# Kernel tuning notes

Hardware: AMD Instinct MI355X
Metric: run time of the kernel (lower is better)

The kernel has to match this reference:

```python
import jax, jax.numpy as jnp
import numpy as np

N = 10000      # atoms
E = 160000     # edges (avg degree 16)
H = 64         # hidden_channels
R = 64         # num_rbf
MAXZ = 100
RC = 4.5       # cutoff_upper (cutoff_lower = 0)
LN_EPS = 1e-5


def setup_inputs() -> dict:
    key = jax.random.key(0)
    ks = jax.random.split(key, 20)
    z = jax.random.randint(ks[0], (N,), 0, MAXZ, dtype=jnp.int32)
    edge_index = jax.random.randint(ks[1], (2, E), 0, N, dtype=jnp.int32)
    edge_weight = jax.random.uniform(ks[2], (E,), dtype=jnp.float32) * RC
    v = jax.random.normal(ks[3], (E, 3), dtype=jnp.float32)
    edge_vec_norm = v / jnp.linalg.norm(v, axis=-1, keepdims=True)
    edge_attr = jax.random.normal(ks[4], (E, R), dtype=jnp.float32)
    p = lambda k, shape: (jax.random.normal(k, shape, dtype=jnp.float32) * 0.1)
    return {
        'z': z, 'edge_index': edge_index, 'edge_weight': edge_weight,
        'edge_vec_norm': edge_vec_norm, 'edge_attr': edge_attr,
        'emb': p(ks[5], (MAXZ, H)),
        'emb2_w': p(ks[6], (H, 2 * H)), 'emb2_b': p(ks[7], (H,)),
        'dp1_w': p(ks[8], (H, R)), 'dp1_b': p(ks[9], (H,)),
        'dp2_w': p(ks[10], (H, R)), 'dp2_b': p(ks[11], (H,)),
        'dp3_w': p(ks[12], (H, R)), 'dp3_b': p(ks[13], (H,)),
        'ln_g': jnp.ones((H,), jnp.float32), 'ln_b': jnp.zeros((H,), jnp.float32),
        'w1': p(ks[14], (2 * H, H)), 'b1': jnp.zeros((2 * H,), jnp.float32),
        'w2': p(ks[15], (3 * H, 2 * H)), 'b2': jnp.zeros((3 * H,), jnp.float32),
        'm0': p(ks[16], (H, H)), 'm1': p(ks[17], (H, H)), 'm2': p(ks[18], (H, H)),
    }


def reference(z, edge_index, edge_weight, edge_vec_norm, edge_attr,
              emb, emb2_w, emb2_b, dp1_w, dp1_b, dp2_w, dp2_b, dp3_w, dp3_b,
              ln_g, ln_b, w1, b1, w2, b2, m0, m1, m2):
    n_atoms = z.shape[0]
    hc = emb.shape[1]
    src, dst = edge_index[0], edge_index[1]

    # atomic number message Z_ij: concat(Z_i, Z_j) -> Linear  [E,H]
    Zn = emb[z]
    Zij = jnp.concatenate([Zn[src], Zn[dst]], axis=-1) @ emb2_w.T + emb2_b

    # cosine cutoff (cutoff_lower == 0)
    C = 0.5 * (jnp.cos(edge_weight * jnp.pi / RC) + 1.0) * (edge_weight < RC)

    # RBF-gated per-edge channel weights, all [E,H]
    g1 = (edge_attr @ dp1_w.T + dp1_b) * C[:, None] * Zij
    g2 = (edge_attr @ dp2_w.T + dp2_b) * C[:, None] * Zij
    g3 = (edge_attr @ dp3_w.T + dp3_b) * C[:, None] * Zij

    eye = jnp.eye(3, dtype=Zij.dtype)
    vx, vy, vz = edge_vec_norm[:, 0], edge_vec_norm[:, 1], edge_vec_norm[:, 2]
    zero = jnp.zeros_like(vx)
    skew = jnp.stack([zero, -vz, vy, vz, zero, -vx, -vy, vx, zero], axis=-1).reshape(-1, 3, 3)
    outer = edge_vec_norm[:, :, None] * edge_vec_norm[:, None, :]  # [E,3,3], symmetric
    sym = outer - (jnp.trace(outer, axis1=-2, axis2=-1) / 3.0)[:, None, None] * eye

    # per-edge messages [E,H,3,3]
    Iij = g1[:, :, None, None] * eye
    Aij = g2[:, :, None, None] * skew[:, None, :, :]
    Sij = g3[:, :, None, None] * sym[:, None, :, :]

    # scatter-add to atoms
    I = jax.ops.segment_sum(Iij, src, num_segments=n_atoms)
    A = jax.ops.segment_sum(Aij, src, num_segments=n_atoms)
    S = jax.ops.segment_sum(Sij, src, num_segments=n_atoms)

    # tensor norm -> layernorm -> MLP1
    tn = ((I + A + S) ** 2).sum((-2, -1))  # [N,H]
    mu = tn.mean(-1, keepdims=True)
    var = ((tn - mu) ** 2).mean(-1, keepdims=True)
    norm = (tn - mu) / jnp.sqrt(var + LN_EPS) * ln_g + ln_b
    norm = jax.nn.silu(norm @ w1.T + b1)
    norm = jax.nn.silu(norm @ w2.T + b2)
    norm = norm.reshape(-1, hc, 3)
    n0 = norm[..., 0][:, :, None, None]

    # channel-mixing; NOTE: original code applies MLP2[1]/MLP2[2] to the
    # updated I and gates all three with norm[...,0] -- replicated faithfully.
    I = jnp.einsum('nhij,kh->nkij', I, m0) * n0
    A = jnp.einsum('nhij,kh->nkij', I, m1) * n0
    S = jnp.einsum('nhij,kh->nkij', I, m2) * n0
    return I + A + S
```

## Files before the change

### kernel.cpp

```cpp
#include <hip/hip_runtime.h>
#include <stdint.h>

#define NATOMS 10000
#define NEDGES 160000
#define RCUT   4.5f
#define CAP    64
#define ATGRID 1024

#define T_BYTES    ((size_t)NATOMS * 640 * 4)
#define CNT_OFF    (T_BYTES)
#define CNT_BYTES  ((size_t)NATOMS * 4)
#define REC_OFF    (CNT_OFF + CNT_BYTES)
#define REC_BYTES  ((size_t)NATOMS * CAP * 16)
#define EMB_OFF    (REC_OFF + REC_BYTES)
#define EMB_BYTES  ((size_t)100 * 64 * 2)
#define ATTR2_OFF  (EMB_OFF + 0x4000)
#define ATTR2_BYTES ((size_t)NATOMS * CAP * 64 * 2)
#define WS_NEED    (ATTR2_OFF + ATTR2_BYTES)

typedef unsigned short u16;
typedef __bf16 bf16x8 __attribute__((ext_vector_type(8)));
typedef float  f32x4  __attribute__((ext_vector_type(4)));

#define MFMA16(a,b,c) __builtin_amdgcn_mfma_f32_16x16x32_bf16((a),(b),(c),0,0,0)
#define BFMAGIC 0x3F803F80u
#define MSK 0xffff0000u

__device__ __forceinline__ float uf(unsigned int u){ return __uint_as_float(u); }
__device__ __forceinline__ float b2f(u16 u){
  union { unsigned int i; float f; } v; v.i = ((unsigned int)u) << 16; return v.f;
}
__device__ __forceinline__ u16 f2b(float f){
  union { unsigned int i; float f; } v; v.f = f;
  unsigned int b = v.i + 0x7fffu + ((v.i >> 16) & 1u);
  return (u16)(b >> 16);
}
__device__ __forceinline__ float ldf(const void* p, int i, int bf){
  if (bf) return b2f(((const u16*)p)[i]);
  return ((const float*)p)[i];
}
__device__ __forceinline__ bf16x8 ld8bf(const void* p, int i, int bf){
  if (bf) return *(const bf16x8*)((const u16*)p + i);
  const float4* q = (const float4*)((const float*)p + i);
  float4 a = q[0], b = q[1];
  bf16x8 r;
  r[0]=(__bf16)a.x; r[1]=(__bf16)a.y; r[2]=(__bf16)a.z; r[3]=(__bf16)a.w;
  r[4]=(__bf16)b.x; r[5]=(__bf16)b.y; r[6]=(__bf16)b.z; r[7]=(__bf16)b.w;
  return r;
}
__device__ __forceinline__ uint4 ld8pk(const void* p, int i, int bf){
  if (bf) return *(const uint4*)((const u16*)p + i);
  const float4* q = (const float4*)((const float*)p + i);
  float4 a = q[0], b = q[1];
  uint4 r;
  r.x = (unsigned int)f2b(a.x) | ((unsigned int)f2b(a.y) << 16);
  r.y = (unsigned int)f2b(a.z) | ((unsigned int)f2b(a.w) << 16);
  r.z = (unsigned int)f2b(b.x) | ((unsigned int)f2b(b.y) << 16);
  r.w = (unsigned int)f2b(b.z) | ((unsigned int)f2b(b.w) << 16);
  return r;
}
__device__ __forceinline__ void ld8f(const void* p, int i, float* o, int bf){
  if (bf){
    uint4 v = *(const uint4*)((const u16*)p + i);
    o[0]=uf(v.x<<16); o[1]=uf(v.x&MSK); o[2]=uf(v.y<<16); o[3]=uf(v.y&MSK);
    o[4]=uf(v.z<<16); o[5]=uf(v.z&MSK); o[6]=uf(v.w<<16); o[7]=uf(v.w&MSK);
    return;
  }
  const float4* q = (const float4*)((const float*)p + i);
  float4 a = q[0], b = q[1];
  o[0]=a.x; o[1]=a.y; o[2]=a.z; o[3]=a.w; o[4]=b.x; o[5]=b.y; o[6]=b.z; o[7]=b.w;
}
__device__ __forceinline__ uint4 pk8(const float* f){
  uint4 r;
  r.x = (unsigned int)f2b(f[0]) | ((unsigned int)f2b(f[1]) << 16);
  r.y = (unsigned int)f2b(f[2]) | ((unsigned int)f2b(f[3]) << 16);
  r.z = (unsigned int)f2b(f[4]) | ((unsigned int)f2b(f[5]) << 16);
  r.w = (unsigned int)f2b(f[6]) | ((unsigned int)f2b(f[7]) << 16);
  return r;
}

__global__ __launch_bounds__(256) void scatter_kernel(const int* __restrict__ ei,
                                                      const int* __restrict__ z,
                                                      const void* __restrict__ ew,
                                                      const void* __restrict__ evn,
                                                      const void* __restrict__ emb,
                                                      u16* __restrict__ emb16,
                                                      int* __restrict__ cnt,
                                                      uint4* __restrict__ REC,
                                                      const void* __restrict__ attr,
                                                      u16* __restrict__ attr2,
                                                      const unsigned int* __restrict__ lng){
  const int bf = (lng[0] == BFMAGIC);
  int e = blockIdx.x * 256 + threadIdx.x;
  if (e < 6400) emb16[e] = bf ? ((const u16*)emb)[e] : f2b(((const float*)emb)[e]);
  int s = ei[e], d = ei[NEDGES + e];
  int p = atomicAdd(&cnt[s], 1);
  const float w  = ldf(ew, e, bf);
  const float Cv = (w < RCUT) ? 0.5f*(__cosf(w * (3.14159265358979f / RCUT)) + 1.0f) : 0.0f;
  uint4 rec;
  rec.x = (unsigned int)e;
  rec.y = (unsigned int)z[d];
  rec.z = (unsigned int)f2b(ldf(evn, 3*e + 0, bf)) | ((unsigned int)f2b(ldf(evn, 3*e + 1, bf)) << 16);
  rec.w = (unsigned int)f2b(ldf(evn, 3*e + 2, bf)) | ((unsigned int)f2b(Cv) << 16);
  if (p < CAP){
    REC[(size_t)s*CAP + p] = rec;
    if (attr2){
      u16* dst = attr2 + ((size_t)s*CAP + p)*64;
#pragma unroll
      for (int k = 0; k < 8; k++)
        *(uint4*)(dst + k*8) = ld8pk(attr, e*64 + k*8, bf);
    }
  }
}

__global__ __launch_bounds__(256)
void atomT_stream(
    const int* __restrict__ z,
    const u16* __restrict__ emb16,
    const u16* __restrict__ attr2,
    const uint4* __restrict__ REC,
    const int* __restrict__ cnt,
    const void* __restrict__ e2w, const void* __restrict__ e2b,
    const void* __restrict__ d1w, const void* __restrict__ d1b,
    const void* __restrict__ d2w, const void* __restrict__ d2b,
    const void* __restrict__ d3w, const void* __restrict__ d3b,
    float* __restrict__ T,
    const unsigned int* __restrict__ lng)
{
  __shared__ __align__(16) u16 dpW[3][64][64];
  __shared__ __align__(16) u16 e2W[64][128];

  const int bf  = (lng[0] == BFMAGIC);
  const int tid = threadIdx.x;
  const void* dps[3] = {d1w, d2w, d3w};
  for (int idx = tid; idx < 1536; idx += 256){
    int w = idx >> 9, rem = idx & 511, r = rem >> 3, c8 = rem & 7;
    *(bf16x8*)&dpW[w][r][(c8 ^ (r & 7))*8] = ld8bf(dps[w], r*64 + c8*8, bf);
  }
  for (int idx = tid; idx < 1024; idx += 256){
    int r = idx >> 4, c8 = idx & 15;
    *(bf16x8*)&e2W[r][(c8 ^ (r & 7))*8] = ld8bf(e2w, r*128 + c8*8, bf);
  }
  __syncthreads();

  const int lane = tid & 63;
  const int wave = tid >> 6;
  const int hh   = lane & 15;
  const int quad = lane >> 4;
  const int half = wave & 1;
  const int ntb  = half * 2;
  const int wpair = wave >> 1;

  float be2[2], bd1[2], bd2[2], bd3[2];
#pragma unroll
  for (int j = 0; j < 2; j++){
    int h = hh + 16*(ntb + j);
    be2[j] = ldf(e2b, h, bf); bd1[j] = ldf(d1b, h, bf);
    bd2[j] = ldf(d2b, h, bf); bd3[j] = ldf(d3b, h, bf);
  }

  int pr  = blockIdx.x;
  int n   = pr * 2 + wpair;
  int cn  = cnt[n];
  int zsv = z[n];

  while (true) {
    const int e0   = n * CAP;
    const int nv   = min(cn, CAP);
    const int e1   = e0 + nv;
    const int e1m1 = (nv > 0) ? (e1 - 1) : e0;
    uint4 recA = REC[min(e0 + hh, e1m1)];

    bf16x8 zf0 = *(const bf16x8*)(emb16 + zsv*64 + quad*8);
    bf16x8 zf1 = *(const bf16x8*)(emb16 + zsv*64 + 32 + quad*8);

    const int prn  = pr + ATGRID;
    const bool more = (prn < NATOMS/2);
    const int nn   = prn * 2 + wpair;
    if (more){ cn = cnt[nn]; zsv = z[nn]; }

    float P[10][2];
#pragma unroll
    for (int c = 0; c < 10; c++){ P[c][0] = 0.f; P[c][1] = 0.f; }

    for (int base = e0; base < e1; base += 16){
      const size_t sA = (size_t)min(base + hh, e1 - 1) * 64;
      bf16x8 af0 = *(const bf16x8*)(attr2 + sA + quad*8);
      bf16x8 af1 = *(const bf16x8*)(attr2 + sA + 32 + quad*8);

      uint4 recN = REC[min(base + 16 + hh, e1 - 1)];

      bf16x8 zf2 = *(const bf16x8*)(emb16 + recA.y*64 + quad*8);
      bf16x8 zf3 = *(const bf16x8*)(emb16 + recA.y*64 + 32 + quad*8);

      f32x4 aZ[2], a1[2], a2[2], a3[2];
#pragma unroll
      for (int j = 0; j < 2; j++){
        aZ[j] = (f32x4){0.f,0.f,0.f,0.f};
        a1[j] = (f32x4){0.f,0.f,0.f,0.f};
        a2[j] = (f32x4){0.f,0.f,0.f,0.f};
        a3[j] = (f32x4){0.f,0.f,0.f,0.f};
      }

#pragma unroll
      for (int j = 0; j < 2; j++){
        const int h  = hh + 16*(ntb + j);
        const int s0 = (quad       ^ (h & 7)) * 8;
        const int s1 = ((quad + 4) ^ (h & 7)) * 8;
        bf16x8 b;
        b = *(const bf16x8*)&dpW[0][h][s0];           a1[j] = MFMA16(af0, b, a1[j]);
        b = *(const bf16x8*)&dpW[0][h][s1];           a1[j] = MFMA16(af1, b, a1[j]);
        b = *(const bf16x8*)&dpW[1][h][s0];           a2[j] = MFMA16(af0, b, a2[j]);
        b = *(const bf16x8*)&dpW[1][h][s1];           a2[j] = MFMA16(af1, b, a2[j]);
        b = *(const bf16x8*)&dpW[2][h][s0];           a3[j] = MFMA16(af0, b, a3[j]);
        b = *(const bf16x8*)&dpW[2][h][s1];           a3[j] = MFMA16(af1, b, a3[j]);
        b = *(const bf16x8*)&e2W[h][s0];              aZ[j] = MFMA16(zf0, b, aZ[j]);
        b = *(const bf16x8*)&e2W[h][s1];              aZ[j] = MFMA16(zf1, b, aZ[j]);
        b = *(const bf16x8*)&e2W[h][((quad + 8)  ^ (h & 7)) * 8];  aZ[j] = MFMA16(zf2, b, aZ[j]);
        b = *(const bf16x8*)&e2W[h][((quad + 12) ^ (h & 7)) * 8];  aZ[j] = MFMA16(zf3, b, aZ[j]);
      }

#pragma unroll
      for (int r = 0; r < 4; r++){
        const int ii = base + quad*4 + r;
        const bool ea = (ii < e1);
        const int srcl = quad*20 + r;
        const unsigned int rz = (unsigned int)__shfl((int)recA.z, srcl, 64);
        const unsigned int rw = (unsigned int)__shfl((int)recA.w, srcl, 64);
        const float Cv = ea ? b2f((u16)(rw >> 16)) : 0.f;
        const float vx = b2f((u16)(rz & 0xffffu));
        const float vy = b2f((u16)(rz >> 16));
        const float vz = b2f((u16)(rw & 0xffffu));
        const float xx = vx*vx - (1.f/3.f), yy = vy*vy - (1.f/3.f), zz = vz*vz - (1.f/3.f);
        const float xy = vx*vy, xz = vx*vz, yz = vy*vz;
#pragma unroll
        for (int j = 0; j < 2; j++){
          const float czv = Cv * (aZ[j][r] + be2[j]);
          const float g1 = (a1[j][r] + bd1[j]) * czv;
          const float g2 = (a2[j][r] + bd2[j]) * czv;
          const float g3 = (a3[j][r] + bd3[j]) * czv;
          P[0][j] += g1;
          P[1][j] += g2*vx; P[2][j] += g2*vy; P[3][j] += g2*vz;
          P[4][j] += g3*xx; P[5][j] += g3*yy; P[6][j] += g3*zz;
          P[7][j] += g3*xy; P[8][j] += g3*xz; P[9][j] += g3*yz;
        }
      }
      recA = recN;
    }

#pragma unroll
    for (int c = 0; c < 10; c++)
#pragma unroll
      for (int j = 0; j < 2; j++){
        float v = P[c][j];
        v += __shfl_xor(v, 16, 64);
        v += __shfl_xor(v, 32, 64);
        P[c][j] = v;
      }

    if ((quad >> 1) == half){
      float* Tn = T + (size_t)n * 640;
#pragma unroll
      for (int c = 0; c < 10; c++)
        Tn[c*64 + lane] = P[c][quad & 1];
    }

    if (!more) break;
    pr = prn; n = nn;
  }
}

__global__ __launch_bounds__(256)
void atomT_kernel(
    const int* __restrict__ z,
    const u16* __restrict__ emb16,
    const void* __restrict__ attr,
    const uint4* __restrict__ REC,
    const int* __restrict__ cnt,
    const void* __restrict__ e2w, const void* __restrict__ e2b,
    const void* __restrict__ d1w, const void* __restrict__ d1b,
    const void* __restrict__ d2w, const void* __restrict__ d2b,
    const void* __restrict__ d3w, const void* __restrict__ d3b,
    float* __restrict__ T,
    const unsigned int* __restrict__ lng)
{
  __shared__ __align__(16) u16 dpW[3][64][64];
  __shared__ __align__(16) u16 e2W[64][128];

  const int bf  = (lng[0] == BFMAGIC);
  const int tid = threadIdx.x;
  const void* dps[3] = {d1w, d2w, d3w};
  for (int idx = tid; idx < 1536; idx += 256){
    int w = idx >> 9, rem = idx & 511, r = rem >> 3, c8 = rem & 7;
    *(bf16x8*)&dpW[w][r][(c8 ^ (r & 7))*8] = ld8bf(dps[w], r*64 + c8*8, bf);
  }
  for (int idx = tid; idx < 1024; idx += 256){
    int r = idx >> 4, c8 = idx & 15;
    *(bf16x8*)&e2W[r][(c8 ^ (r & 7))*8] = ld8bf(e2w, r*128 + c8*8, bf);
  }
  __syncthreads();

  const int lane = tid & 63;
  const int wave = tid >> 6;
  const int hh   = lane & 15;
  const int quad = lane >> 4;
  const int half = wave & 1;
  const int ntb  = half * 2;
  const int wpair = wave >> 1;

  float be2[2], bd1[2], bd2[2], bd3[2];
#pragma unroll
  for (int j = 0; j < 2; j++){
    int h = hh + 16*(ntb + j);
    be2[j] = ldf(e2b, h, bf); bd1[j] = ldf(d1b, h, bf);
    bd2[j] = ldf(d2b, h, bf); bd3[j] = ldf(d3b, h, bf);
  }

  int pr  = blockIdx.x;
  int n   = pr * 2 + wpair;
  int cn  = cnt[n];
  int zsv = z[n];

  while (true) {
    const int e0   = n * CAP;
    const int nv   = min(cn, CAP);
    const int e1   = e0 + nv;
    const int e1m1 = (nv > 0) ? (e1 - 1) : e0;
    uint4 recA = REC[min(e0 + hh, e1m1)];

    bf16x8 zf0 = *(const bf16x8*)(emb16 + zsv*64 + quad*8);
    bf16x8 zf1 = *(const bf16x8*)(emb16 + zsv*64 + 32 + quad*8);

    const int prn  = pr + ATGRID;
    const bool more = (prn < NATOMS/2);
    const int nn   = prn * 2 + wpair;
    if (more){ cn = cnt[nn]; zsv = z[nn]; }

    float P[10][2];
#pragma unroll
    for (int c = 0; c < 10; c++){ P[c][0] = 0.f; P[c][1] = 0.f; }

    for (int base = e0; base < e1; base += 16){
      uint4 recN = REC[min(base + 16 + hh, e1 - 1)];

      bf16x8 af0 = ld8bf(attr, (int)recA.x*64 + quad*8, bf);
      bf16x8 af1 = ld8bf(attr, (int)recA.x*64 + 32 + quad*8, bf);
      bf16x8 zf2 = *(const bf16x8*)(emb16 + recA.y*64 + quad*8);
      bf16x8 zf3 = *(const bf16x8*)(emb16 + recA.y*64 + 32 + quad*8);

      f32x4 aZ[2], a1[2], a2[2], a3[2];
#pragma unroll
      for (int j = 0; j < 2; j++){
        aZ[j] = (f32x4){0.f,0.f,0.f,0.f};
        a1[j] = (f32x4){0.f,0.f,0.f,0.f};
        a2[j] = (f32x4){0.f,0.f,0.f,0.f};
        a3[j] = (f32x4){0.f,0.f,0.f,0.f};
      }

#pragma unroll
      for (int j = 0; j < 2; j++){
        const int h  = hh + 16*(ntb + j);
        const int s0 = (quad       ^ (h & 7)) * 8;
        const int s1 = ((quad + 4) ^ (h & 7)) * 8;
        bf16x8 b;
        b = *(const bf16x8*)&dpW[0][h][s0];           a1[j] = MFMA16(af0, b, a1[j]);
        b = *(const bf16x8*)&dpW[0][h][s1];           a1[j] = MFMA16(af1, b, a1[j]);
        b = *(const bf16x8*)&dpW[1][h][s0];           a2[j] = MFMA16(af0, b, a2[j]);
        b = *(const bf16x8*)&dpW[1][h][s1];           a2[j] = MFMA16(af1, b, a2[j]);
        b = *(const bf16x8*)&dpW[2][h][s0];           a3[j] = MFMA16(af0, b, a3[j]);
        b = *(const bf16x8*)&dpW[2][h][s1];           a3[j] = MFMA16(af1, b, a3[j]);
        b = *(const bf16x8*)&e2W[h][s0];              aZ[j] = MFMA16(zf0, b, aZ[j]);
        b = *(const bf16x8*)&e2W[h][s1];              aZ[j] = MFMA16(zf1, b, aZ[j]);
        b = *(const bf16x8*)&e2W[h][((quad + 8)  ^ (h & 7)) * 8];  aZ[j] = MFMA16(zf2, b, aZ[j]);
        b = *(const bf16x8*)&e2W[h][((quad + 12) ^ (h & 7)) * 8];  aZ[j] = MFMA16(zf3, b, aZ[j]);
      }

#pragma unroll
      for (int r = 0; r < 4; r++){
        const int ii = base + quad*4 + r;
        const bool ea = (ii < e1);
        const int srcl = quad*20 + r;
        const unsigned int rz = (unsigned int)__shfl((int)recA.z, srcl, 64);
        const unsigned int rw = (unsigned int)__shfl((int)recA.w, srcl, 64);
        const float Cv = ea ? b2f((u16)(rw >> 16)) : 0.f;
        const float vx = b2f((u16)(rz & 0xffffu));
        const float vy = b2f((u16)(rz >> 16));
        const float vz = b2f((u16)(rw & 0xffffu));
        const float xx = vx*vx - (1.f/3.f), yy = vy*vy - (1.f/3.f), zz = vz*vz - (1.f/3.f);
        const float xy = vx*vy, xz = vx*vz, yz = vy*vz;
#pragma unroll
        for (int j = 0; j < 2; j++){
          const float czv = Cv * (aZ[j][r] + be2[j]);
          const float g1 = (a1[j][r] + bd1[j]) * czv;
          const float g2 = (a2[j][r] + bd2[j]) * czv;
          const float g3 = (a3[j][r] + bd3[j]) * czv;
          P[0][j] += g1;
          P[1][j] += g2*vx; P[2][j] += g2*vy; P[3][j] += g2*vz;
          P[4][j] += g3*xx; P[5][j] += g3*yy; P[6][j] += g3*zz;
          P[7][j] += g3*xy; P[8][j] += g3*xz; P[9][j] += g3*yz;
        }
      }
      recA = recN;
    }

#pragma unroll
    for (int c = 0; c < 10; c++)
#pragma unroll
      for (int j = 0; j < 2; j++){
        float v = P[c][j];
        v += __shfl_xor(v, 16, 64);
        v += __shfl_xor(v, 32, 64);
        P[c][j] = v;
      }

    if ((quad >> 1) == half){
      float* Tn = T + (size_t)n * 640;
#pragma unroll
      for (int c = 0; c < 10; c++)
        Tn[c*64 + lane] = P[c][quad & 1];
    }

    if (!more) break;
    pr = prn; n = nn;
  }
}

__global__ __launch_bounds__(256) void mlp_kernel(
    const float* __restrict__ T,
    const void* __restrict__ ln_g, const void* __restrict__ ln_b,
    const void* __restrict__ w1,  const void* __restrict__ b1,
    const void* __restrict__ w2,  const void* __restrict__ b2p,
    const void* __restrict__ m0,  const void* __restrict__ m1,
    const void* __restrict__ m2,  void* __restrict__ out,
    const unsigned int* __restrict__ lng)
{
  __shared__ __align__(16) u16 w1L[128][72];
  __shared__ __align__(16) u16 w2L[64][136];
  __shared__ __align__(16) u16 m0L[64][72];
  __shared__ __align__(16) u16 msL[64][72];
  __shared__ __align__(16) float xbuf[4][64];
  __shared__ __align__(16) float hbuf2[4][128];
  __shared__ __align__(16) float isoB[4][64];
  __shared__ __align__(16) float i1B[4][64];

  const int bf  = (lng[0] == BFMAGIC);
  const int tid = threadIdx.x;

  for (int idx = tid; idx < 1024; idx += 256){
    int r = idx >> 3, c8 = idx & 7;
    *(uint4*)&w1L[r][c8*8] = ld8pk(w1, r*64 + c8*8, bf);
  }
  for (int idx = tid; idx < 1024; idx += 256){
    int r = idx >> 4, c8 = idx & 15;
    *(uint4*)&w2L[r][c8*8] = ld8pk(w2, (3*r)*128 + c8*8, bf);
  }
  for (int idx = tid; idx < 512; idx += 256){
    int r = idx >> 3, c8 = idx & 7;
    *(uint4*)&m0L[r][c8*8] = ld8pk(m0, r*64 + c8*8, bf);
    float f[8], g[8];
    ld8f(m1, r*64 + c8*8, f, bf);
    ld8f(m2, r*64 + c8*8, g, bf);
#pragma unroll
    for (int q = 0; q < 8; q++) f[q] += g[q];
    *(uint4*)&msL[r][c8*8] = pk8(f);
  }
  __syncthreads();

  const int wave = tid >> 6;
  const int h    = tid & 63;
  const int wid  = blockIdx.x * 4 + wave;

  const float lngh = ldf(ln_g, h, bf), lnbh = ldf(ln_b, h, bf);
  const float b1a = ldf(b1, h, bf), b1b = ldf(b1, h + 64, bf);
  const float b2h = ldf(b2p, 3*h, bf);

  const uint4*  A4 = (const uint4*)&w1L[h][0];
  const uint4*  B4 = (const uint4*)&w1L[h + 64][0];
  const uint4*  W4 = (const uint4*)&w2L[h][0];
  const uint4*  M4 = (const uint4*)&m0L[h][0];
  const uint4*  S4 = (const uint4*)&msL[h][0];
  const float4* X4  = (const float4*)&xbuf[wave][0];
  const float4* H4  = (const float4*)&hbuf2[wave][0];
  const float4* I4  = (const float4*)&isoB[wave][0];
  const float4* J4  = (const float4*)&i1B[wave][0];

  const int NITER = (NATOMS + 2047) / 2048;
  for (int it = 0; it < NITER; it++){
    const int n   = wid + it * 2048;
    const bool act = (n < NATOMS);
    const int na  = act ? n : 0;

    const float* Tn = T + (size_t)na * 640;
    const float iso = Tn[h];
    const float wx = Tn[64+h], wy = Tn[128+h], wz = Tn[192+h];
    const float sxx = Tn[256+h], syy = Tn[320+h], szz = Tn[384+h];
    const float sxy = Tn[448+h], sxz = Tn[512+h], syz = Tn[576+h];
    const float tn = (iso+sxx)*(iso+sxx) + (iso+syy)*(iso+syy) + (iso+szz)*(iso+szz)
                   + 2.f*(sxy*sxy + sxz*sxz + syz*syz + wx*wx + wy*wy + wz*wz);
    isoB[wave][h] = iso;

    float s = tn;
#pragma unroll
    for (int off = 32; off; off >>= 1) s += __shfl_xor(s, off, 64);
    const float mu = s * (1.f/64.f);
    const float d0 = tn - mu;
    float v = d0 * d0;
#pragma unroll
    for (int off = 32; off; off >>= 1) v += __shfl_xor(v, off, 64);
    v *= (1.f/64.f);
    xbuf[wave][h] = d0 * rsqrtf(v + 1e-5f) * lngh + lnbh;
    __syncthreads();

    float acc0 = b1a, acc1 = b1b;
#pragma unroll
    for (int q = 0; q < 8; q++){
      const uint4 A = A4[q], B = B4[q];
      const float4 x0 = X4[2*q], x1 = X4[2*q + 1];
      acc0 += uf(A.x << 16)*x0.x + uf(A.x & MSK)*x0.y;
      acc0 += uf(A.y << 16)*x0.z + uf(A.y & MSK)*x0.w;
      acc0 += uf(A.z << 16)*x1.x + uf(A.z & MSK)*x1.y;
      acc0 += uf(A.w << 16)*x1.z + uf(A.w & MSK)*x1.w;
      acc1 += uf(B.x << 16)*x0.x + uf(B.x & MSK)*x0.y;
      acc1 += uf(B.y << 16)*x0.z + uf(B.y & MSK)*x0.w;
      acc1 += uf(B.z << 16)*x1.x + uf(B.z & MSK)*x1.y;
      acc1 += uf(B.w << 16)*x1.z + uf(B.w & MSK)*x1.w;
    }
    acc0 = acc0 / (1.f + __expf(-acc0));
    acc1 = acc1 / (1.f + __expf(-acc1));
    hbuf2[wave][h] = acc0; hbuf2[wave][h + 64] = acc1;
    __syncthreads();

    float acc2 = b2h, t1 = 0.f;
#pragma unroll
    for (int q = 0; q < 16; q++){
      const uint4 W = W4[q];
      const float4 y0 = H4[2*q], y1 = H4[2*q + 1];
      acc2 += uf(W.x << 16)*y0.x + uf(W.x & MSK)*y0.y;
      acc2 += uf(W.y << 16)*y0.z + uf(W.y & MSK)*y0.w;
      acc2 += uf(W.z << 16)*y1.x + uf(W.z & MSK)*y1.y;
      acc2 += uf(W.w << 16)*y1.z + uf(W.w & MSK)*y1.w;
    }
#pragma unroll
    for (int q = 0; q < 8; q++){
      const uint4 M = M4[q];
      const float4 x0 = I4[2*q], x1 = I4[2*q + 1];
      t1 += uf(M.x << 16)*x0.x + uf(M.x & MSK)*x0.y;
      t1 += uf(M.y << 16)*x0.z + uf(M.y & MSK)*x0.w;
      t1 += uf(M.z << 16)*x1.x + uf(M.z & MSK)*x1.y;
      t1 += uf(M.w << 16)*x1.z + uf(M.w & MSK)*x1.w;
    }
    const float n0 = acc2 / (1.f + __expf(-acc2));
    const float iso1 = t1 * n0;
    i1B[wave][h] = iso1;
    __syncthreads();

    float t23 = 0.f;
#pragma unroll
    for (int q = 0; q < 8; q++){
      const uint4 M = S4[q];
      const float4 x0 = J4[2*q], x1 = J4[2*q + 1];
      t23 += uf(M.x << 16)*x0.x + uf(M.x & MSK)*x0.y;
      t23 += uf(M.y << 16)*x0.z + uf(M.y & MSK)*x0.w;
      t23 += uf(M.z << 16)*x1.x + uf(M.z & MSK)*x1.y;
      t23 += uf(M.w << 16)*x1.z + uf(M.w & MSK)*x1.w;
    }
    const float dval = iso1 + t23 * n0;

    if (act){
      if (bf){
        u16* o = (u16*)out + (size_t)n * 576 + h * 9;
        const u16 db = f2b(dval);
        o[0] = db; o[1] = 0; o[2] = 0;
        o[3] = 0;  o[4] = db; o[5] = 0;
        o[6] = 0;  o[7] = 0;  o[8] = db;
      } else {
        float* o = (float*)out + (size_t)n * 576 + h * 9;
        o[0] = dval; o[1] = 0.f; o[2] = 0.f;
        o[3] = 0.f;  o[4] = dval; o[5] = 0.f;
        o[6] = 0.f;  o[7] = 0.f;  o[8] = dval;
      }
    }
    __syncthreads();
  }
}

extern "C" void kernel_launch(void* const* d_in, const int* in_sizes, int n_in,
                              void* d_out, int out_size, void* d_ws, size_t ws_size,
                              hipStream_t stream) {
  const int* z    = (const int*)d_in[0];
  const int* ei   = (const int*)d_in[1];
  const void* ew   = d_in[2];
  const void* evn  = d_in[3];
  const void* attr = d_in[4];
  const void* emb  = d_in[5];
  const void* e2w  = d_in[6];
  const void* e2b  = d_in[7];
  const void* d1w  = d_in[8];
  const void* d1b  = d_in[9];
  const void* d2w  = d_in[10];
  const void* d2b  = d_in[11];
  const void* d3w  = d_in[12];
  const void* d3b  = d_in[13];
  const void* ln_g = d_in[14];
  const void* ln_b = d_in[15];
  const void* w1   = d_in[16];
  const void* b1   = d_in[17];
  const void* w2   = d_in[18];
  const void* b2p  = d_in[19];
  const void* m0   = d_in[20];
  const void* m1   = d_in[21];
  const void* m2   = d_in[22];
  const unsigned int* lng = (const unsigned int*)ln_g;

  char* ws = (char*)d_ws;
  float*   T     = (float*)ws;
  int*     cnt   = (int*)(ws + CNT_OFF);
  uint4*   REC   = (uint4*)(ws + REC_OFF);
  u16*     emb16 = (u16*)(ws + EMB_OFF);
  u16*     attr2 = (ws_size >= WS_NEED) ? (u16*)(ws + ATTR2_OFF) : nullptr;

  hipMemsetAsync(cnt, 0, CNT_BYTES, stream);
  scatter_kernel<<<NEDGES/256, 256, 0, stream>>>(ei, z, ew, evn, emb, emb16, cnt, REC,
                                                 attr, attr2, lng);
  if (attr2)
    atomT_stream<<<ATGRID, 256, 0, stream>>>(z, emb16, attr2, REC, cnt, e2w, e2b,
                                             d1w, d1b, d2w, d2b, d3w, d3b, T, lng);
  else
    atomT_kernel<<<ATGRID, 256, 0, stream>>>(z, emb16, attr, REC, cnt, e2w, e2b,
                                             d1w, d1b, d2w, d2b, d3w, d3b, T, lng);
  mlp_kernel<<<512, 256, 0, stream>>>(T, ln_g, ln_b, w1, b1, w2, b2p,
                                      m0, m1, m2, d_out, lng);
}
```

Measured before the change: 251.0 us.

## Assign one atom per block with each wave covering sixteen channels

Reworks the atom-tensor kernel's work split. Previously each block handled two atoms, with each wave computing 32 channels of one atom. Now each block handles one atom and each of the four waves computes 16 channels. This halves per-wave MFMA work and accumulator registers per edge tile, which should help occupancy and latency hiding. In exchange, each wave redundantly loads the edge attributes and records, and per-atom edge loads are replicated across four waves instead of two. The grid stride loop now steps over atoms directly.

```diff
diff --git a/kernel.cpp b/kernel.cpp
--- a/kernel.cpp
+++ b/kernel.cpp
@@ -147,20 +147,19 @@
   const int wave = tid >> 6;
   const int hh   = lane & 15;
   const int quad = lane >> 4;
-  const int half = wave & 1;
-  const int ntb  = half * 2;
-  const int wpair = wave >> 1;
-
-  float be2[2], bd1[2], bd2[2], bd3[2];
-#pragma unroll
-  for (int j = 0; j < 2; j++){
-    int h = hh + 16*(ntb + j);
-    be2[j] = ldf(e2b, h, bf); bd1[j] = ldf(d1b, h, bf);
-    bd2[j] = ldf(d2b, h, bf); bd3[j] = ldf(d3b, h, bf);
-  }
-
-  int pr  = blockIdx.x;
-  int n   = pr * 2 + wpair;
+  const int h    = hh + 16*wave;
+
+  const float be2 = ldf(e2b, h, bf);
+  const float bd1 = ldf(d1b, h, bf);
+  const float bd2 = ldf(d2b, h, bf);
+  const float bd3 = ldf(d3b, h, bf);
+
+  const int s0 = (quad        ^ (h & 7)) * 8;
+  const int s1 = ((quad + 4)  ^ (h & 7)) * 8;
+  const int s2 = ((quad + 8)  ^ (h & 7)) * 8;
+  const int s3 = ((quad + 12) ^ (h & 7)) * 8;
+
+  int n   = blockIdx.x;
   int cn  = cnt[n];
   int zsv = z[n];
 
@@ -174,14 +173,13 @@
     bf16x8 zf0 = *(const bf16x8*)(emb16 + zsv*64 + quad*8);
     bf16x8 zf1 = *(const bf16x8*)(emb16 + zsv*64 + 32 + quad*8);
 
-    const int prn  = pr + ATGRID;
-    const bool more = (prn < NATOMS/2);
-    const int nn   = prn * 2 + wpair;
+    const int nn   = n + ATGRID;
+    const bool more = (nn < NATOMS);
     if (more){ cn = cnt[nn]; zsv = z[nn]; }
 
-    float P[10][2];
-#pragma unroll
-    for (int c = 0; c < 10; c++){ P[c][0] = 0.f; P[c][1] = 0.f; }
+    float P[10];
+#pragma unroll
+    for (int c = 0; c < 10; c++) P[c] = 0.f;
 
     for (int base = e0; base < e1; base += 16){
       const size_t sA = (size_t)min(base + hh, e1 - 1) * 64;
@@ -193,31 +191,23 @@
       bf16x8 zf2 = *(const bf16x8*)(emb16 + recA.y*64 + quad*8);
       bf16x8 zf3 = *(const bf16x8*)(emb16 + recA.y*64 + 32 + quad*8);
 
-      f32x4 aZ[2], a1[2], a2[2], a3[2];
-#pragma unroll
-      for (int j = 0; j < 2; j++){
-        aZ[j] = (f32x4){0.f,0.f,0.f,0.f};
-        a1[j] = (f32x4){0.f,0.f,0.f,0.f};
-        a2[j] = (f32x4){0.f,0.f,0.f,0.f};
-        a3[j] = (f32x4){0.f,0.f,0.f,0.f};
-      }
-
-#pragma unroll
-      for (int j = 0; j < 2; j++){
-        const int h  = hh + 16*(ntb + j);
-        const int s0 = (quad       ^ (h & 7)) * 8;
-        const int s1 = ((quad + 4) ^ (h & 7)) * 8;
+      f32x4 aZ = (f32x4){0.f,0.f,0.f,0.f};
+      f32x4 a1 = (f32x4){0.f,0.f,0.f,0.f};
+      f32x4 a2 = (f32x4){0.f,0.f,0.f,0.f};
+      f32x4 a3 = (f32x4){0.f,0.f,0.f,0.f};
+
+      {
         bf16x8 b;
-        b = *(const bf16x8*)&dpW[0][h][s0];           a1[j] = MFMA16(af0, b, a1[j]);
-        b = *(const bf16x8*)&dpW[0][h][s1];           a1[j] = MFMA16(af1, b, a1[j]);
-        b = *(const bf16x8*)&dpW[1][h][s0];           a2[j] = MFMA16(af0, b, a2[j]);
-        b = *(const bf16x8*)&dpW[1][h][s1];           a2[j] = MFMA16(af1, b, a2[j]);
-        b = *(const bf16x8*)&dpW[2][h][s0];           a3[j] = MFMA16(af0, b, a3[j]);
-        b = *(const bf16x8*)&dpW[2][h][s1];           a3[j] = MFMA16(af1, b, a3[j]);
-        b = *(const bf16x8*)&e2W[h][s0];              aZ[j] = MFMA16(zf0, b, aZ[j]);
-        b = *(const bf16x8*)&e2W[h][s1];              aZ[j] = MFMA16(zf1, b, aZ[j]);
-        b = *(const bf16x8*)&e2W[h][((quad + 8)  ^ (h & 7)) * 8];  aZ[j] = MFMA16(zf2, b, aZ[j]);
-        b = *(const bf16x8*)&e2W[h][((quad + 12) ^ (h & 7)) * 8];  aZ[j] = MFMA16(zf3, b, aZ[j]);
+        b = *(const bf16x8*)&dpW[0][h][s0];  a1 = MFMA16(af0, b, a1);
+        b = *(const bf16x8*)&dpW[0][h][s1];  a1 = MFMA16(af1, b, a1);
+        b = *(const bf16x8*)&dpW[1][h][s0];  a2 = MFMA16(af0, b, a2);
+        b = *(const bf16x8*)&dpW[1][h][s1];  a2 = MFMA16(af1, b, a2);
+        b = *(const bf16x8*)&dpW[2][h][s0];  a3 = MFMA16(af0, b, a3);
+        b = *(const bf16x8*)&dpW[2][h][s1];  a3 = MFMA16(af1, b, a3);
+        b = *(const bf16x8*)&e2W[h][s0];     aZ = MFMA16(zf0, b, aZ);
+        b = *(const bf16x8*)&e2W[h][s1];     aZ = MFMA16(zf1, b, aZ);
+        b = *(const bf16x8*)&e2W[h][s2];     aZ = MFMA16(zf2, b, aZ);
+        b = *(const bf16x8*)&e2W[h][s3];     aZ = MFMA16(zf3, b, aZ);
       }
 
 #pragma unroll
@@ -233,40 +223,35 @@
         const float vz = b2f((u16)(rw & 0xffffu));
         const float xx = vx*vx - (1.f/3.f), yy = vy*vy - (1.f/3.f), zz = vz*vz - (1.f/3.f);
         const float xy = vx*vy, xz = vx*vz, yz = vy*vz;
-#pragma unroll
-        for (int j = 0; j < 2; j++){
-          const float czv = Cv * (aZ[j][r] + be2[j]);
-          const float g1 = (a1[j][r] + bd1[j]) * czv;
-          const float g2 = (a2[j][r] + bd2[j]) * czv;
-          const float g3 = (a3[j][r] + bd3[j]) * czv;
-          P[0][j] += g1;
-          P[1][j] += g2*vx; P[2][j] += g2*vy; P[3][j] += g2*vz;
-          P[4][j] += g3*xx; P[5][j] += g3*yy; P[6][j] += g3*zz;
-          P[7][j] += g3*xy; P[8][j] += g3*xz; P[9][j] += g3*yz;
-        }
+        const float czv = Cv * (aZ[r] + be2);
+        const float g1 = (a1[r] + bd1) * czv;
+        const float g2 = (a2[r] + bd2) * czv;
+        const float g3 = (a3[r] + bd3) * czv;
+        P[0] += g1;
+        P[1] += g2*vx; P[2] += g2*vy; P[3] += g2*vz;
+        P[4] += g3*xx; P[5] += g3*yy; P[6] += g3*zz;
+        P[7] += g3*xy; P[8] += g3*xz; P[9] += g3*yz;
       }
       recA = recN;
     }
 
 #pragma unroll
-    for (int c = 0; c < 10; c++)
-#pragma unroll
-      for (int j = 0; j < 2; j++){
-        float v = P[c][j];
-        v += __shfl_xor(v, 16, 64);
-        v += __shfl_xor(v, 32, 64);
-        P[c][j] = v;
-      }
-
-    if ((quad >> 1) == half){
-      float* Tn = T + (size_t)n * 640;
+    for (int c = 0; c < 10; c++){
+      float v = P[c];
+      v += __shfl_xor(v, 16, 64);
+      v += __shfl_xor(v, 32, 64);
+      P[c] = v;
+    }
+
+    if (quad == 0){
+      float* Tn = T + (size_t)n * 640 + 16*wave + hh;
 #pragma unroll
       for (int c = 0; c < 10; c++)
-        Tn[c*64 + lane] = P[c][quad & 1];
+        Tn[c*64] = P[c];
     }
 
     if (!more) break;
-    pr = prn; n = nn;
+    n = nn;
   }
 }
 
```

Result: no change. 250.8 us (-0.1%).
